# Kernel tuning notes

Hardware: AMD Instinct MI355X
Metric: run time of the kernel (lower is better)

The kernel has to match this reference:

```python
import jax, jax.numpy as jnp
import numpy as np

B, C, H, W = 32, 1024, 28, 28
TEXT_DIM = 768
ATTN_DIM = 256
REDUCTION = 16
RED = max(1, C // REDUCTION)


def setup_inputs() -> dict:
    key = jax.random.key(0)
    ks = jax.random.split(key, 8)
    x = jax.random.normal(ks[0], (B, C, H, W), dtype=jnp.float32)
    text_feat = jax.random.normal(ks[1], (B, TEXT_DIM), dtype=jnp.float32)
    # ChannelAttention shared MLP (Linear weights, torch layout [out, in], no bias)
    w1 = jax.random.normal(ks[2], (RED, C), dtype=jnp.float32) * (1.0 / np.sqrt(C))
    w2 = jax.random.normal(ks[3], (C, RED), dtype=jnp.float32) * (1.0 / np.sqrt(RED))
    # TextGuidedSpatialAttention projections
    wq = jax.random.normal(ks[4], (ATTN_DIM, TEXT_DIM), dtype=jnp.float32) * 0.001
    wk = jax.random.normal(ks[5], (ATTN_DIM, C), dtype=jnp.float32) * np.sqrt(2.0 / ATTN_DIM)
    wv = jax.random.normal(ks[6], (ATTN_DIM, C), dtype=jnp.float32) * np.sqrt(2.0 / ATTN_DIM)
    wo = jax.random.normal(ks[7], (1, ATTN_DIM), dtype=jnp.float32) * np.sqrt(2.0)
    return {"x": x, "text_feat": text_feat, "w1": w1, "w2": w2,
            "wq": wq, "wk": wk, "wv": wv, "wo": wo}


def _forward(x, text_feat, w1, w2, wq, wk, wv, wo):
    b, c, h, w = x.shape
    # ----- Channel attention -----
    avg = jnp.mean(x, axis=(2, 3))          # [B, C]
    mx = jnp.max(x, axis=(2, 3))            # [B, C]
    def mlp(z):
        return jax.nn.relu(z @ w1.T) @ w2.T  # [B, C]
    ch_attn = jax.nn.sigmoid(mlp(avg) + mlp(mx))   # [B, C]
    x = x * ch_attn[:, :, None, None]
    # ----- Text-guided spatial attention -----
    q = text_feat @ wq.T                     # [B, A]
    # 1x1 conv == channel contraction
    k = jnp.einsum('ac,bchw->bahw', wk, x).reshape(b, ATTN_DIM, h * w)  # [B, A, N]
    v = jnp.einsum('ac,bchw->bahw', wv, x).reshape(b, ATTN_DIM, h * w)  # [B, A, N]
    scores = jnp.einsum('ba,ban->bn', q, k) / jnp.sqrt(jnp.float32(ATTN_DIM))  # [B, N]
    attn_weights = jax.nn.softmax(scores, axis=-1)                      # [B, N]
    attended = jnp.einsum('bn,ban->ba', attn_weights, v)                # [B, A]
    # out_proj 1x1 conv on a spatially-constant tensor == scalar per batch, broadcast
    spatial_scalar = jax.nn.sigmoid(attended @ wo.T)                    # [B, 1]
    spatial_attn = jnp.broadcast_to(spatial_scalar[:, :, None, None], (b, 1, h, w))
    return x * spatial_attn, spatial_attn


def reference(x, text_feat, w1, w2, wq, wk, wv, wo):
    return _forward(x, text_feat, w1, w2, wq, wk, wv, wo)
```

## Files before the change

kernel.cpp:

```cpp
#include <hip/hip_runtime.h>
#include <math.h>

#define B_   32
#define C_   1024
#define N_   784
#define NF4  196
#define TD   768
#define AD   256
#define RED_ 64
#define OUT0 25690112
#define ROWS (B_*C_)
#define CH_  16
#define CPB  64

typedef float f4 __attribute__((ext_vector_type(4)));

#define OFF_AVG  0
#define OFF_MAX  32768
#define OFF_CA   65536
#define OFF_Q    98304
#define OFF_HS   106496
#define OFF_WVO  108544
#define OFF_GQ   109568
#define OFF_SV   142336
#define OFF_CNT  142368
#define OFF_PS   142400
#define OFF_PY   543808

__global__ void k_avgmax(const float* __restrict__ x, const float* __restrict__ text,
                         const float* __restrict__ wq, float* __restrict__ avg,
                         float* __restrict__ mx, float* __restrict__ q,
                         int* __restrict__ cnt) {
    int blk = blockIdx.x;
    int wave = threadIdx.x >> 6, lane = threadIdx.x & 63;
    if (blk < 4096) {
        int row0 = blk * 8 + wave * 2;
        const float4* r0 = (const float4*)(x + (size_t)row0 * N_);
        const float4* r1 = r0 + NF4;
        float s0 = 0.f, s1 = 0.f, m0 = -3.4e38f, m1 = -3.4e38f;
        #pragma unroll
        for (int j = 0; j < 3; ++j) {
            int i = lane + 64 * j;
            float4 v0 = r0[i], v1 = r1[i];
            s0 += v0.x + v0.y + v0.z + v0.w;
            s1 += v1.x + v1.y + v1.z + v1.w;
            m0 = fmaxf(m0, fmaxf(fmaxf(v0.x, v0.y), fmaxf(v0.z, v0.w)));
            m1 = fmaxf(m1, fmaxf(fmaxf(v1.x, v1.y), fmaxf(v1.z, v1.w)));
        }
        if (lane < 4) {
            float4 v0 = r0[192 + lane], v1 = r1[192 + lane];
            s0 += v0.x + v0.y + v0.z + v0.w;
            s1 += v1.x + v1.y + v1.z + v1.w;
            m0 = fmaxf(m0, fmaxf(fmaxf(v0.x, v0.y), fmaxf(v0.z, v0.w)));
            m1 = fmaxf(m1, fmaxf(fmaxf(v1.x, v1.y), fmaxf(v1.z, v1.w)));
        }
        for (int o = 32; o; o >>= 1) {
            s0 += __shfl_down(s0, o, 64);
            s1 += __shfl_down(s1, o, 64);
            m0 = fmaxf(m0, __shfl_down(m0, o, 64));
            m1 = fmaxf(m1, __shfl_down(m1, o, 64));
        }
        if (lane == 0) {
            avg[row0]     = s0 * (1.f / (float)N_); mx[row0]     = m0;
            avg[row0 + 1] = s1 * (1.f / (float)N_); mx[row0 + 1] = m1;
        }
    } else if (blk < 6144) {
        int w = (blk - 4096) * 4 + wave;
        int b = w >> 8, a = w & 255;
        const float4* tb = (const float4*)(text + (size_t)b * TD);
        const float4* wr = (const float4*)(wq + (size_t)a * TD);
        float acc = 0.f;
        #pragma unroll
        for (int j = 0; j < 3; ++j) {
            int i = lane + 64 * j;
            float4 tv = tb[i], wvv = wr[i];
            acc += tv.x * wvv.x + tv.y * wvv.y + tv.z * wvv.z + tv.w * wvv.w;
        }
        for (int o = 32; o; o >>= 1) acc += __shfl_down(acc, o, 64);
        if (lane == 0) q[(size_t)b * AD + a] = acc;
    } else {
        if (threadIdx.x < B_) cnt[threadIdx.x] = 0;
    }
}

__global__ void k_proj(const float* __restrict__ avg, const float* __restrict__ mx,
                       const float* __restrict__ w1, const float* __restrict__ q,
                       const float* __restrict__ wk, const float* __restrict__ wv,
                       const float* __restrict__ wo, float* __restrict__ hs,
                       float* __restrict__ gq, float* __restrict__ wvo) {
    int blk  = blockIdx.x;
    int wave = threadIdx.x >> 6, lane = threadIdx.x & 63;
    int t = threadIdx.x;
    __shared__ float red[256];
    __shared__ float qs[AD];
    if (blk < 512) {
        int w = blk * 4 + wave;
        int b = w >> 6, r = w & 63;
        const float4* av = (const float4*)(avg + (size_t)b * C_);
        const float4* mv = (const float4*)(mx + (size_t)b * C_);
        const float4* wr = (const float4*)(w1 + (size_t)r * C_);
        float aa = 0.f, am = 0.f;
        #pragma unroll
        for (int j = 0; j < 4; ++j) {
            int i = lane + 64 * j;
            float4 wvv = wr[i], a4 = av[i], m4 = mv[i];
            aa += wvv.x * a4.x + wvv.y * a4.y + wvv.z * a4.z + wvv.w * a4.w;
            am += wvv.x * m4.x + wvv.y * m4.y + wvv.z * m4.z + wvv.w * m4.w;
        }
        for (int o = 32; o; o >>= 1) {
            aa += __shfl_down(aa, o, 64);
            am += __shfl_down(am, o, 64);
        }
        if (lane == 0) hs[(size_t)b * RED_ + r] = fmaxf(aa, 0.f) + fmaxf(am, 0.f);
    } else if (blk < 1024) {
        int local = blk - 512;
        int b  = local >> 4, cb = local & 15;
        int cl = t & 63, sl = t >> 6;
        int c  = cb * 64 + cl;
        qs[t] = q[(size_t)b * AD + t];
        __syncthreads();
        const float* wkp = wk + (size_t)(sl * 64) * C_ + c;
        float acc = 0.f;
        #pragma unroll 8
        for (int a = 0; a < 64; ++a) acc += qs[sl * 64 + a] * wkp[(size_t)a * C_];
        red[t] = acc;
        __syncthreads();
        if (t < 64) gq[(size_t)b * C_ + c] = red[t] + red[64 + t] + red[128 + t] + red[192 + t];
    } else {
        int local = blk - 1024;
        int cl = t & 63, sl = t >> 6;
        int c = local * 64 + cl;
        const float* wvp = wv + (size_t)(sl * 64) * C_ + c;
        float acc = 0.f;
        #pragma unroll 8
        for (int a = 0; a < 64; ++a) acc += wo[sl * 64 + a] * wvp[(size_t)a * C_];
        red[t] = acc;
        __syncthreads();
        if (t < 64) wvo[local * 64 + t] = red[t] + red[64 + t] + red[128 + t] + red[192 + t];
    }
}

__global__ __launch_bounds__(256) void k_scores(
        const float* __restrict__ x, const float* __restrict__ hs,
        const float* __restrict__ w2, const float* __restrict__ gq,
        const float* __restrict__ wvo,
        float* __restrict__ ca, float* __restrict__ partS, float* __restrict__ partY,
        int* __restrict__ cnt, float* __restrict__ sv) {
    int chunk = blockIdx.x, b = blockIdx.y, t = threadIdx.x;
    int wave = t >> 6, lane = t & 63;
    __shared__ float hss[RED_];
    __shared__ float redB[256];
    __shared__ float gsg[CPB], gsh[CPB];
    __shared__ float4 l4s[4 * NF4], l4y[4 * NF4];
    __shared__ float rm[4], rs[4], rd[4];
    __shared__ int winflag;

    if (t < RED_) hss[t] = hs[(size_t)b * RED_ + t];
    __syncthreads();
    {
        int cl = t & 63, sl = t >> 6;
        int c  = chunk * CPB + cl;
        const float* w2p = w2 + (size_t)c * RED_ + sl * 16;
        float a1 = 0.f;
        #pragma unroll
        for (int r = 0; r < 16; ++r) a1 += hss[sl * 16 + r] * w2p[r];
        redB[t] = a1;
    }
    __syncthreads();
    if (t < CPB) {
        float s1 = redB[t] + redB[64 + t] + redB[128 + t] + redB[192 + t];
        float cav = 1.f / (1.f + __expf(-s1));
        int c = chunk * CPB + t;
        ca[(size_t)b * C_ + c] = cav;
        gsg[t] = gq[(size_t)b * C_ + c] * cav * 0.0625f;
        gsh[t] = wvo[c] * cav;
    }
    __syncthreads();
    const float4* xb4 = (const float4*)(x +
        ((size_t)b * C_ + (size_t)chunk * CPB + (size_t)wave * 16) * N_);
    float4 z = make_float4(0.f, 0.f, 0.f, 0.f);
    float4 s0 = z, s1v = z, s2v = z, s3 = z;
    float4 y0 = z, y1 = z, y2 = z, y3 = z;
    #pragma unroll 4
    for (int cc = 0; cc < 16; ++cc) {
        float gv = gsg[wave * 16 + cc], hv = gsh[wave * 16 + cc];
        const float4* row = xb4 + (size_t)cc * NF4;
        float4 v;
        v = row[lane];
        s0.x += gv*v.x; s0.y += gv*v.y; s0.z += gv*v.z; s0.w += gv*v.w;
        y0.x += hv*v.x; y0.y += hv*v.y; y0.z += hv*v.z; y0.w += hv*v.w;
        v = row[lane + 64];
        s1v.x += gv*v.x; s1v.y += gv*v.y; s1v.z += gv*v.z; s1v.w += gv*v.w;
        y1.x  += hv*v.x; y1.y  += hv*v.y; y1.z  += hv*v.z; y1.w  += hv*v.w;
        v = row[lane + 128];
        s2v.x += gv*v.x; s2v.y += gv*v.y; s2v.z += gv*v.z; s2v.w += gv*v.w;
        y2.x  += hv*v.x; y2.y  += hv*v.y; y2.z  += hv*v.z; y2.w  += hv*v.w;
        if (lane < 4) {
            v = row[lane + 192];
            s3.x += gv*v.x; s3.y += gv*v.y; s3.z += gv*v.z; s3.w += gv*v.w;
            y3.x += hv*v.x; y3.y += hv*v.y; y3.z += hv*v.z; y3.w += hv*v.w;
        }
    }
    l4s[wave * NF4 + lane]       = s0;
    l4s[wave * NF4 + lane + 64]  = s1v;
    l4s[wave * NF4 + lane + 128] = s2v;
    l4y[wave * NF4 + lane]       = y0;
    l4y[wave * NF4 + lane + 64]  = y1;
    l4y[wave * NF4 + lane + 128] = y2;
    if (lane < 4) {
        l4s[wave * NF4 + lane + 192] = s3;
        l4y[wave * NF4 + lane + 192] = y3;
    }
    __syncthreads();
    if (t < NF4) {
        float4 a = l4s[t], bb = l4s[NF4 + t], c4 = l4s[2 * NF4 + t], d = l4s[3 * NF4 + t];
        float4 r;
        r.x = a.x + bb.x + c4.x + d.x; r.y = a.y + bb.y + c4.y + d.y;
        r.z = a.z + bb.z + c4.z + d.z; r.w = a.w + bb.w + c4.w + d.w;
        ((float4*)(partS + ((size_t)b * CH_ + chunk) * N_))[t] = r;
        a = l4y[t]; bb = l4y[NF4 + t]; c4 = l4y[2 * NF4 + t]; d = l4y[3 * NF4 + t];
        r.x = a.x + bb.x + c4.x + d.x; r.y = a.y + bb.y + c4.y + d.y;
        r.z = a.z + bb.z + c4.z + d.z; r.w = a.w + bb.w + c4.w + d.w;
        ((float4*)(partY + ((size_t)b * CH_ + chunk) * N_))[t] = r;
    }
    __syncthreads();
    if (t == 0) {
        __threadfence();
        winflag = (atomicAdd(&cnt[b], 1) == CH_ - 1) ? 1 : 0;
    }
    __syncthreads();
    if (!winflag) return;
    __threadfence();
    const float* pS = partS + (size_t)b * CH_ * N_;
    const float* pY = partY + (size_t)b * CH_ * N_;
    float v0 = 0.f, v1 = 0.f, v2 = 0.f, v3 = 0.f;
    float w0 = 0.f, w1v = 0.f, w2v = 0.f, w3 = 0.f;
    for (int ch = 0; ch < CH_; ++ch) {
        const float* pcs = pS + (size_t)ch * N_;
        const float* pcy = pY + (size_t)ch * N_;
        v0 += pcs[t]; v1 += pcs[t + 256]; v2 += pcs[t + 512];
        w0 += pcy[t]; w1v += pcy[t + 256]; w2v += pcy[t + 512];
        if (t < 16) { v3 += pcs[t + 768]; w3 += pcy[t + 768]; }
    }
    float m = fmaxf(fmaxf(v0, v1), v2);
    if (t < 16) m = fmaxf(m, v3);
    for (int o = 32; o; o >>= 1) m = fmaxf(m, __shfl_down(m, o, 64));
    if (lane == 0) rm[wave] = m;
    __syncthreads();
    float M = fmaxf(fmaxf(rm[0], rm[1]), fmaxf(rm[2], rm[3]));
    float e0 = __expf(v0 - M), e1 = __expf(v1 - M), e2 = __expf(v2 - M);
    float e3 = (t < 16) ? __expf(v3 - M) : 0.f;
    float ssum = e0 + e1 + e2 + e3;
    float dot  = e0 * w0 + e1 * w1v + e2 * w2v + e3 * w3;
    for (int o = 32; o; o >>= 1) {
        ssum += __shfl_down(ssum, o, 64);
        dot  += __shfl_down(dot,  o, 64);
    }
    if (lane == 0) { rs[wave] = ssum; rd[wave] = dot; }
    __syncthreads();
    if (t == 0) {
        float S = rs[0] + rs[1] + rs[2] + rs[3];
        float D = rd[0] + rd[1] + rd[2] + rd[3];
        sv[b] = 1.f / (1.f + __expf(-D / S));
    }
}

__global__ void k_finalize(const float* __restrict__ x, const float* __restrict__ chattn,
                           const float* __restrict__ s, float* __restrict__ out) {
    int blk = blockIdx.x;
    if (blk < ROWS / 8) {
        int wave = threadIdx.x >> 6, lane = threadIdx.x & 63;
        int row0 = blk * 8 + wave * 2;
        int b    = row0 >> 10;
        float sb  = s[b];
        float sc0 = chattn[row0] * sb;
        float sc1 = chattn[row0 + 1] * sb;
        const float4* r0 = (const float4*)(x + (size_t)row0 * N_);
        const float4* r1 = r0 + NF4;
        f4* o0 = (f4*)(out + (size_t)row0 * N_);
        f4* o1 = o0 + NF4;
        #pragma unroll
        for (int j = 0; j < 3; ++j) {
            int i = lane + 64 * j;
            float4 v0 = r0[i], v1 = r1[i];
            f4 w0 = { v0.x * sc0, v0.y * sc0, v0.z * sc0, v0.w * sc0 };
            f4 w1 = { v1.x * sc1, v1.y * sc1, v1.z * sc1, v1.w * sc1 };
            __builtin_nontemporal_store(w0, &o0[i]);
            __builtin_nontemporal_store(w1, &o1[i]);
        }
        if (lane < 4) {
            int i = 192 + lane;
            float4 v0 = r0[i], v1 = r1[i];
            f4 w0 = { v0.x * sc0, v0.y * sc0, v0.z * sc0, v0.w * sc0 };
            f4 w1 = { v1.x * sc1, v1.y * sc1, v1.z * sc1, v1.w * sc1 };
            __builtin_nontemporal_store(w0, &o0[i]);
            __builtin_nontemporal_store(w1, &o1[i]);
        }
    } else {
        int idx = (blk - ROWS / 8) * 256 + threadIdx.x;
        if (idx < (B_ * N_) / 4) {
            int b = idx / (N_ / 4);
            float v = s[b];
            f4 vv = { v, v, v, v };
            __builtin_nontemporal_store(vv, &((f4*)(out + OUT0))[idx]);
        }
    }
}

extern "C" void kernel_launch(void* const* d_in, const int* in_sizes, int n_in,
                              void* d_out, int out_size, void* d_ws, size_t ws_size,
                              hipStream_t stream) {
    const float* x    = (const float*)d_in[0];
    const float* text = (const float*)d_in[1];
    const float* w1   = (const float*)d_in[2];
    const float* w2   = (const float*)d_in[3];
    const float* wq   = (const float*)d_in[4];
    const float* wk   = (const float*)d_in[5];
    const float* wv   = (const float*)d_in[6];
    const float* wo   = (const float*)d_in[7];
    float* out = (float*)d_out;
    float* ws  = (float*)d_ws;

    float* avg   = ws + OFF_AVG;
    float* mx    = ws + OFF_MAX;
    float* ca    = ws + OFF_CA;
    float* q     = ws + OFF_Q;
    float* hs    = ws + OFF_HS;
    float* wvo   = ws + OFF_WVO;
    float* gq    = ws + OFF_GQ;
    float* sv    = ws + OFF_SV;
    int*   cnt   = (int*)(ws + OFF_CNT);
    float* partS = ws + OFF_PS;
    float* partY = ws + OFF_PY;

    k_avgmax<<<6145, 256, 0, stream>>>(x, text, wq, avg, mx, q, cnt);
    k_proj<<<1040, 256, 0, stream>>>(avg, mx, w1, q, wk, wv, wo, hs, gq, wvo);
    k_scores<<<dim3(CH_, B_), 256, 0, stream>>>(x, hs, w2, gq, wvo, ca, partS, partY, cnt, sv);
    k_finalize<<<ROWS / 8 + 25, 256, 0, stream>>>(x, ca, sv, out);
}
```

Before: 260.6 us.

## Split score kernel over spatial halves and reduce partials with atomics

The scores kernel now runs on twice as many blocks, each handling half of the spatial positions for a 64-channel chunk. This gives more parallelism and fewer idle lanes per wave. Per-chunk partial buffers are replaced by float atomicAdd into per-batch S and Y accumulators, which the first kernel zeroes, so the last block reads one reduced row instead of summing 16 partials. Launch bounds now request higher occupancy. The cost is atomic contention and nondeterministic float summation order, and the channel-attention MLP is computed twice per chunk.

```diff
diff --git a/kernel.cpp b/kernel.cpp
--- a/kernel.cpp
+++ b/kernel.cpp
@@ -15,22 +15,23 @@
 
 typedef float f4 __attribute__((ext_vector_type(4)));
 
-#define OFF_AVG  0
-#define OFF_MAX  32768
-#define OFF_CA   65536
-#define OFF_Q    98304
-#define OFF_HS   106496
-#define OFF_WVO  108544
-#define OFF_GQ   109568
-#define OFF_SV   142336
-#define OFF_CNT  142368
-#define OFF_PS   142400
-#define OFF_PY   543808
+#define OFF_AVG 0
+#define OFF_MAX 32768
+#define OFF_CA  65536
+#define OFF_Q   98304
+#define OFF_HS  106496
+#define OFF_WVO 108544
+#define OFF_GQ  109568
+#define OFF_SV  142336
+#define OFF_CNT 142368
+#define OFF_S   142400
+#define OFF_Y   167488
 
 __global__ void k_avgmax(const float* __restrict__ x, const float* __restrict__ text,
                          const float* __restrict__ wq, float* __restrict__ avg,
                          float* __restrict__ mx, float* __restrict__ q,
-                         int* __restrict__ cnt) {
+                         int* __restrict__ cnt, float* __restrict__ S,
+                         float* __restrict__ Y) {
     int blk = blockIdx.x;
     int wave = threadIdx.x >> 6, lane = threadIdx.x & 63;
     if (blk < 4096) {
@@ -78,6 +79,12 @@
         }
         for (int o = 32; o; o >>= 1) acc += __shfl_down(acc, o, 64);
         if (lane == 0) q[(size_t)b * AD + a] = acc;
+    } else if (blk < 6169) {
+        int idx = (blk - 6144) * 256 + threadIdx.x;
+        if (idx < 6272) {
+            f4 z = {0.f, 0.f, 0.f, 0.f};
+            ((f4*)S)[idx] = z; ((f4*)Y)[idx] = z;
+        }
     } else {
         if (threadIdx.x < B_) cnt[threadIdx.x] = 0;
     }
@@ -140,18 +147,21 @@
     }
 }
 
-__global__ __launch_bounds__(256) void k_scores(
+__global__ __launch_bounds__(256, 4) void k_scores(
         const float* __restrict__ x, const float* __restrict__ hs,
         const float* __restrict__ w2, const float* __restrict__ gq,
         const float* __restrict__ wvo,
-        float* __restrict__ ca, float* __restrict__ partS, float* __restrict__ partY,
+        float* __restrict__ ca, float* __restrict__ S, float* __restrict__ Y,
         int* __restrict__ cnt, float* __restrict__ sv) {
-    int chunk = blockIdx.x, b = blockIdx.y, t = threadIdx.x;
+    int chunk = blockIdx.x;
+    int bh    = blockIdx.y;
+    int b = bh >> 1, half = bh & 1;
+    int t = threadIdx.x;
     int wave = t >> 6, lane = t & 63;
     __shared__ float hss[RED_];
     __shared__ float redB[256];
     __shared__ float gsg[CPB], gsh[CPB];
-    __shared__ float4 l4s[4 * NF4], l4y[4 * NF4];
+    __shared__ f4 l4s[392], l4y[392];
     __shared__ float rm[4], rs[4], rd[4];
     __shared__ int winflag;
 
@@ -176,80 +186,54 @@
         gsh[t] = wvo[c] * cav;
     }
     __syncthreads();
-    const float4* xb4 = (const float4*)(x +
-        ((size_t)b * C_ + (size_t)chunk * CPB + (size_t)wave * 16) * N_);
-    float4 z = make_float4(0.f, 0.f, 0.f, 0.f);
-    float4 s0 = z, s1v = z, s2v = z, s3 = z;
-    float4 y0 = z, y1 = z, y2 = z, y3 = z;
+    const f4* xb4 = (const f4*)(x +
+        ((size_t)b * C_ + (size_t)chunk * CPB + (size_t)wave * 16) * N_) + (size_t)half * 98;
+    f4 sA = {0,0,0,0}, sB = {0,0,0,0}, yA = {0,0,0,0}, yB = {0,0,0,0};
     #pragma unroll 4
     for (int cc = 0; cc < 16; ++cc) {
         float gv = gsg[wave * 16 + cc], hv = gsh[wave * 16 + cc];
-        const float4* row = xb4 + (size_t)cc * NF4;
-        float4 v;
-        v = row[lane];
-        s0.x += gv*v.x; s0.y += gv*v.y; s0.z += gv*v.z; s0.w += gv*v.w;
-        y0.x += hv*v.x; y0.y += hv*v.y; y0.z += hv*v.z; y0.w += hv*v.w;
-        v = row[lane + 64];
-        s1v.x += gv*v.x; s1v.y += gv*v.y; s1v.z += gv*v.z; s1v.w += gv*v.w;
-        y1.x  += hv*v.x; y1.y  += hv*v.y; y1.z  += hv*v.z; y1.w  += hv*v.w;
-        v = row[lane + 128];
-        s2v.x += gv*v.x; s2v.y += gv*v.y; s2v.z += gv*v.z; s2v.w += gv*v.w;
-        y2.x  += hv*v.x; y2.y  += hv*v.y; y2.z  += hv*v.z; y2.w  += hv*v.w;
-        if (lane < 4) {
-            v = row[lane + 192];
-            s3.x += gv*v.x; s3.y += gv*v.y; s3.z += gv*v.z; s3.w += gv*v.w;
-            y3.x += hv*v.x; y3.y += hv*v.y; y3.z += hv*v.z; y3.w += hv*v.w;
-        }
-    }
-    l4s[wave * NF4 + lane]       = s0;
-    l4s[wave * NF4 + lane + 64]  = s1v;
-    l4s[wave * NF4 + lane + 128] = s2v;
-    l4y[wave * NF4 + lane]       = y0;
-    l4y[wave * NF4 + lane + 64]  = y1;
-    l4y[wave * NF4 + lane + 128] = y2;
-    if (lane < 4) {
-        l4s[wave * NF4 + lane + 192] = s3;
-        l4y[wave * NF4 + lane + 192] = y3;
-    }
-    __syncthreads();
-    if (t < NF4) {
-        float4 a = l4s[t], bb = l4s[NF4 + t], c4 = l4s[2 * NF4 + t], d = l4s[3 * NF4 + t];
-        float4 r;
-        r.x = a.x + bb.x + c4.x + d.x; r.y = a.y + bb.y + c4.y + d.y;
-        r.z = a.z + bb.z + c4.z + d.z; r.w = a.w + bb.w + c4.w + d.w;
-        ((float4*)(partS + ((size_t)b * CH_ + chunk) * N_))[t] = r;
-        a = l4y[t]; bb = l4y[NF4 + t]; c4 = l4y[2 * NF4 + t]; d = l4y[3 * NF4 + t];
-        r.x = a.x + bb.x + c4.x + d.x; r.y = a.y + bb.y + c4.y + d.y;
-        r.z = a.z + bb.z + c4.z + d.z; r.w = a.w + bb.w + c4.w + d.w;
-        ((float4*)(partY + ((size_t)b * CH_ + chunk) * N_))[t] = r;
+        const f4* row = xb4 + (size_t)cc * NF4;
+        f4 v = row[lane];
+        sA += gv * v; yA += hv * v;
+        if (lane < 34) {
+            f4 v2 = row[64 + lane];
+            sB += gv * v2; yB += hv * v2;
+        }
+    }
+    l4s[wave * 98 + lane] = sA; l4y[wave * 98 + lane] = yA;
+    if (lane < 34) { l4s[wave * 98 + 64 + lane] = sB; l4y[wave * 98 + 64 + lane] = yB; }
+    __syncthreads();
+    if (t < 98) {
+        f4 rsv = l4s[t] + l4s[98 + t] + l4s[196 + t] + l4s[294 + t];
+        f4 ryv = l4y[t] + l4y[98 + t] + l4y[196 + t] + l4y[294 + t];
+        float* Sp = S + (size_t)b * N_ + half * 392 + t * 4;
+        float* Yp = Y + (size_t)b * N_ + half * 392 + t * 4;
+        atomicAdd(Sp + 0, rsv.x); atomicAdd(Sp + 1, rsv.y);
+        atomicAdd(Sp + 2, rsv.z); atomicAdd(Sp + 3, rsv.w);
+        atomicAdd(Yp + 0, ryv.x); atomicAdd(Yp + 1, ryv.y);
+        atomicAdd(Yp + 2, ryv.z); atomicAdd(Yp + 3, ryv.w);
     }
     __syncthreads();
     if (t == 0) {
         __threadfence();
-        winflag = (atomicAdd(&cnt[b], 1) == CH_ - 1) ? 1 : 0;
+        winflag = (atomicAdd(&cnt[b], 1) == 2 * CH_ - 1) ? 1 : 0;
     }
     __syncthreads();
     if (!winflag) return;
     __threadfence();
-    const float* pS = partS + (size_t)b * CH_ * N_;
-    const float* pY = partY + (size_t)b * CH_ * N_;
-    float v0 = 0.f, v1 = 0.f, v2 = 0.f, v3 = 0.f;
-    float w0 = 0.f, w1v = 0.f, w2v = 0.f, w3 = 0.f;
-    for (int ch = 0; ch < CH_; ++ch) {
-        const float* pcs = pS + (size_t)ch * N_;
-        const float* pcy = pY + (size_t)ch * N_;
-        v0 += pcs[t]; v1 += pcs[t + 256]; v2 += pcs[t + 512];
-        w0 += pcy[t]; w1v += pcy[t + 256]; w2v += pcy[t + 512];
-        if (t < 16) { v3 += pcs[t + 768]; w3 += pcy[t + 768]; }
-    }
-    float m = fmaxf(fmaxf(v0, v1), v2);
-    if (t < 16) m = fmaxf(m, v3);
+    const float* Sb = S + (size_t)b * N_;
+    const float* Yb = Y + (size_t)b * N_;
+    float v0 = Sb[t], v1 = Sb[t + 256], v2 = Sb[t + 512];
+    float v3 = (t < 16) ? Sb[t + 768] : -3.4e38f;
+    float m = fmaxf(fmaxf(v0, v1), fmaxf(v2, v3));
     for (int o = 32; o; o >>= 1) m = fmaxf(m, __shfl_down(m, o, 64));
     if (lane == 0) rm[wave] = m;
     __syncthreads();
     float M = fmaxf(fmaxf(rm[0], rm[1]), fmaxf(rm[2], rm[3]));
     float e0 = __expf(v0 - M), e1 = __expf(v1 - M), e2 = __expf(v2 - M);
     float e3 = (t < 16) ? __expf(v3 - M) : 0.f;
+    float w0 = Yb[t], w1v = Yb[t + 256], w2v = Yb[t + 512];
+    float w3 = (t < 16) ? Yb[t + 768] : 0.f;
     float ssum = e0 + e1 + e2 + e3;
     float dot  = e0 * w0 + e1 * w1v + e2 * w2v + e3 * w3;
     for (int o = 32; o; o >>= 1) {
@@ -259,9 +243,9 @@
     if (lane == 0) { rs[wave] = ssum; rd[wave] = dot; }
     __syncthreads();
     if (t == 0) {
-        float S = rs[0] + rs[1] + rs[2] + rs[3];
-        float D = rd[0] + rd[1] + rd[2] + rd[3];
-        sv[b] = 1.f / (1.f + __expf(-D / S));
+        float Ssum = rs[0] + rs[1] + rs[2] + rs[3];
+        float Dsum = rd[0] + rd[1] + rd[2] + rd[3];
+        sv[b] = 1.f / (1.f + __expf(-Dsum / Ssum));
     }
 }
 
@@ -321,20 +305,20 @@
     float* out = (float*)d_out;
     float* ws  = (float*)d_ws;
 
-    float* avg   = ws + OFF_AVG;
-    float* mx    = ws + OFF_MAX;
-    float* ca    = ws + OFF_CA;
-    float* q     = ws + OFF_Q;
-    float* hs    = ws + OFF_HS;
-    float* wvo   = ws + OFF_WVO;
-    float* gq    = ws + OFF_GQ;
-    float* sv    = ws + OFF_SV;
-    int*   cnt   = (int*)(ws + OFF_CNT);
-    float* partS = ws + OFF_PS;
-    float* partY = ws + OFF_PY;
-
-    k_avgmax<<<6145, 256, 0, stream>>>(x, text, wq, avg, mx, q, cnt);
+    float* avg = ws + OFF_AVG;
+    float* mx  = ws + OFF_MAX;
+    float* ca  = ws + OFF_CA;
+    float* q   = ws + OFF_Q;
+    float* hs  = ws + OFF_HS;
+    float* wvo = ws + OFF_WVO;
+    float* gq  = ws + OFF_GQ;
+    float* sv  = ws + OFF_SV;
+    int*   cnt = (int*)(ws + OFF_CNT);
+    float* S   = ws + OFF_S;
+    float* Y   = ws + OFF_Y;
+
+    k_avgmax<<<6170, 256, 0, stream>>>(x, text, wq, avg, mx, q, cnt, S, Y);
     k_proj<<<1040, 256, 0, stream>>>(avg, mx, w1, q, wk, wv, wo, hs, gq, wvo);
-    k_scores<<<dim3(CH_, B_), 256, 0, stream>>>(x, hs, w2, gq, wvo, ca, partS, partY, cnt, sv);
+    k_scores<<<dim3(CH_, B_ * 2), 256, 0, stream>>>(x, hs, w2, gq, wvo, ca, S, Y, cnt, sv);
     k_finalize<<<ROWS / 8 + 25, 256, 0, stream>>>(x, ca, sv, out);
 }
```

New measurement: 264.3 us. Within noise of the previous version (+1.4%).
